# Kernel optimization log

Measured on AMD Instinct MI355X. Metric: run time of the kernel, lower is better.

The kernel has to match this reference:

```python
import jax, jax.numpy as jnp
import numpy as np

K_NEIGHBORS = 32  # nsample

def setup_inputs() -> dict:
    key = jax.random.key(0)
    ks = jax.random.split(key, 16)
    B, C, N = 4, 3, 4096
    def w(k, shape):
        return jax.random.normal(k, shape, dtype=jnp.float32) * 0.05
    inp = {"x": jax.random.normal(ks[0], (B, C, N), dtype=jnp.float32)}
    # three scale MLPs share shapes -> stack along leading scale axis (s=3)
    inp["sW0"] = w(ks[1], (3, 64, 3));    inp["sb0"] = w(ks[2], (3, 64))
    inp["sW1"] = w(ks[3], (3, 64, 64));   inp["sb1"] = w(ks[4], (3, 64))
    inp["sW2"] = w(ks[5], (3, 128, 64));  inp["sb2"] = w(ks[6], (3, 128))
    inp["gW0"] = w(ks[7], (256, 384));    inp["gb0"] = w(ks[8], (256,))
    inp["gW1"] = w(ks[9], (1024, 256));   inp["gb1"] = w(ks[10], (1024,))
    inp["mW0"] = w(ks[11], (256, 1024));  inp["mb0"] = w(ks[12], (256,))
    inp["mW1"] = w(ks[13], (128, 256));   inp["mb1"] = w(ks[14], (128,))
    return inp

def _knn_idx(x, k):
    # x: [B, 3, N] channels-first points; k nearest neighbors excluding self
    pts = jnp.swapaxes(x, 1, 2)                       # [B, N, 3]
    sq = jnp.sum(pts * pts, axis=-1)                  # [B, N]
    d = sq[:, :, None] + sq[:, None, :] - 2.0 * jnp.einsum('bnc,bmc->bnm', pts, pts)
    _, idx = jax.lax.top_k(-d, k + 1)                 # nearest first (self at 0)
    return idx[:, :, 1:]                              # [B, N, k]

def reference(x, sW0, sb0, sW1, sb1, sW2, sb2, gW0, gb0, gW1, gb1, mW0, mb0, mW1, mb1):
    B, C, N = x.shape
    # radius is unused by sample_and_group_knn -> all three scales share knn idx
    idx = _knn_idx(x, K_NEIGHBORS)                    # [B, N, K]
    # gather: per-batch x[:, idx[b]] -> [B, C, N, K]
    g = jax.vmap(lambda xf, i: xf[:, i])(x, idx)
    # three shared-weight 1x1-conv MLPs, batched over scale axis s
    h = jax.nn.relu(jnp.einsum('bcnk,soc->sbonk', g, sW0) + sb0[:, None, :, None, None])
    h = jax.nn.relu(jnp.einsum('sbcnk,soc->sbonk', h, sW1) + sb1[:, None, :, None, None])
    h = jax.nn.relu(jnp.einsum('sbcnk,soc->sbonk', h, sW2) + sb2[:, None, :, None, None])
    p = jnp.max(h, axis=-1)                           # [3, B, 128, N] max over neighbors
    point = jnp.moveaxis(p, 0, 1).reshape(B, 3 * p.shape[2], N)  # concat scales -> [B, 384, N]
    gf = jax.nn.relu(jnp.einsum('bcn,oc->bon', point, gW0) + gb0[None, :, None])
    gf = jax.nn.relu(jnp.einsum('bcn,oc->bon', gf, gW1) + gb1[None, :, None])     # [B,1024,N]
    msf = jax.nn.relu(jnp.einsum('bcn,oc->bon', gf, mW0) + mb0[None, :, None])
    msf = jax.nn.relu(jnp.einsum('bcn,oc->bon', msf, mW1) + mb1[None, :, None])   # [B,128,N]
    global_feature = jnp.max(gf, axis=-1)             # [B, 1024]
    return (global_feature, msf)
```

## Files before the change

### kernel.cpp

```cpp
#include <hip/hip_runtime.h>
#include <hip/hip_bf16.h>

#define NPTS 4096
#define KNN  32

typedef __attribute__((ext_vector_type(8))) short short8;
typedef __attribute__((ext_vector_type(4))) float floatx4;
typedef unsigned short u16x2 __attribute__((ext_vector_type(2)));

__device__ __forceinline__ unsigned short f2bf(float f) {
    unsigned u = __float_as_uint(f);
    u = (u + 0x7FFFu + ((u >> 16) & 1u)) >> 16;
    return (unsigned short)u;
}

__global__ __launch_bounds__(256) void prep_all(
    const float* __restrict__ x, float4* __restrict__ pts4,
    const float* __restrict__ gW0, const float* __restrict__ gW1,
    const float* __restrict__ mW0, const float* __restrict__ mW1,
    const float* __restrict__ sW1, const float* __restrict__ sW2,
    unsigned short* __restrict__ Wb0, unsigned short* __restrict__ Wb1,
    unsigned short* __restrict__ Wb2, unsigned short* __restrict__ Wb3,
    unsigned short* __restrict__ Wb4, unsigned short* __restrict__ Wb5)
{
    const int blk = blockIdx.x, t = threadIdx.x;
    if (blk < 64) {
        const int i = blk * 256 + t;
        const int b = i >> 12, n = i & (NPTS - 1);
        const float* xb = x + (size_t)b * 3 * NPTS;
        const float qx = xb[n], qy = xb[NPTS + n], qz = xb[2 * NPTS + n];
        pts4[i] = make_float4(qx, qy, qz, qx * qx + qy * qy + qz * qz);
    } else {
        const int wi = (blk - 64) * 256 + t;
        float v; unsigned short* dst;
        if (wi < 98304)       { v = gW0[wi];          dst = Wb0 + wi; }
        else if (wi < 360448) { v = gW1[wi - 98304];  dst = Wb1 + (wi - 98304); }
        else if (wi < 622592) { v = mW0[wi - 360448]; dst = Wb2 + (wi - 360448); }
        else if (wi < 655360) { v = mW1[wi - 622592]; dst = Wb3 + (wi - 622592); }
        else if (wi < 667648) { v = sW1[wi - 655360]; dst = Wb4 + (wi - 655360); }
        else                  { v = sW2[wi - 667648]; dst = Wb5 + (wi - 667648); }
        *dst = f2bf(v);
    }
}

__global__ __launch_bounds__(256) void knn_kernel19(const float4* __restrict__ pts4,
                                                    int* __restrict__ knn_out)
{
    __shared__ unsigned sredA[2][4], sredB[2][4];
    __shared__ unsigned minSA[256], minSB[256];
    __shared__ unsigned long long CA[256], CB[256];
    __shared__ unsigned ccnt2[2];

    const int t = threadIdx.x, wid = t >> 6, lane = t & 63;
    const int pr = blockIdx.x;
    const int b  = pr >> 11;
    const int qa = ((pr & 2047) << 1);
    const int qb = qa + 1;
    const float4* P = pts4 + ((size_t)b << 12);
    const float4 sA = P[qa];
    const float4 sB = P[qb];

    if (t < 2) ccnt2[t] = 0u;
    CA[t] = 0xFFFFFFFFFFFFFFFFULL;
    CB[t] = 0xFFFFFFFFFFFFFFFFULL;

    unsigned kA[16], kB[16];
    #pragma unroll
    for (int g = 0; g < 4; ++g) {
        float4 c0 = P[((g * 4 + 0) << 8) + t];
        float4 c1 = P[((g * 4 + 1) << 8) + t];
        float4 c2 = P[((g * 4 + 2) << 8) + t];
        float4 c3 = P[((g * 4 + 3) << 8) + t];
        float dA0 = (sA.w + c0.w) - 2.0f * (sA.x * c0.x + sA.y * c0.y + sA.z * c0.z);
        float dA1 = (sA.w + c1.w) - 2.0f * (sA.x * c1.x + sA.y * c1.y + sA.z * c1.z);
        float dA2 = (sA.w + c2.w) - 2.0f * (sA.x * c2.x + sA.y * c2.y + sA.z * c2.z);
        float dA3 = (sA.w + c3.w) - 2.0f * (sA.x * c3.x + sA.y * c3.y + sA.z * c3.z);
        float dB0 = (sB.w + c0.w) - 2.0f * (sB.x * c0.x + sB.y * c0.y + sB.z * c0.z);
        float dB1 = (sB.w + c1.w) - 2.0f * (sB.x * c1.x + sB.y * c1.y + sB.z * c1.z);
        float dB2 = (sB.w + c2.w) - 2.0f * (sB.x * c2.x + sB.y * c2.y + sB.z * c2.z);
        float dB3 = (sB.w + c3.w) - 2.0f * (sB.x * c3.x + sB.y * c3.y + sB.z * c3.z);
        unsigned uA0 = __float_as_uint(dA0), uA1 = __float_as_uint(dA1);
        unsigned uA2 = __float_as_uint(dA2), uA3 = __float_as_uint(dA3);
        unsigned uB0 = __float_as_uint(dB0), uB1 = __float_as_uint(dB1);
        unsigned uB2 = __float_as_uint(dB2), uB3 = __float_as_uint(dB3);
        kA[g * 4 + 0] = uA0 ^ (((unsigned)((int)uA0 >> 31)) | 0x80000000u);
        kA[g * 4 + 1] = uA1 ^ (((unsigned)((int)uA1 >> 31)) | 0x80000000u);
        kA[g * 4 + 2] = uA2 ^ (((unsigned)((int)uA2 >> 31)) | 0x80000000u);
        kA[g * 4 + 3] = uA3 ^ (((unsigned)((int)uA3 >> 31)) | 0x80000000u);
        kB[g * 4 + 0] = uB0 ^ (((unsigned)((int)uB0 >> 31)) | 0x80000000u);
        kB[g * 4 + 1] = uB1 ^ (((unsigned)((int)uB1 >> 31)) | 0x80000000u);
        kB[g * 4 + 2] = uB2 ^ (((unsigned)((int)uB2 >> 31)) | 0x80000000u);
        kB[g * 4 + 3] = uB3 ^ (((unsigned)((int)uB3 >> 31)) | 0x80000000u);
    }

    unsigned tmA = kA[0], tmB = kB[0];
    #pragma unroll
    for (int r = 1; r < 16; ++r) {
        tmA = (kA[r] < tmA) ? kA[r] : tmA;
        tmB = (kB[r] < tmB) ? kB[r] : tmB;
    }
    minSA[t] = tmA;
    minSB[t] = tmB;
    __syncthreads();

    unsigned mA = minSA[lane], mB = minSB[lane];
    {
        unsigned a1 = minSA[lane + 64], a2 = minSA[lane + 128], a3 = minSA[lane + 192];
        unsigned b1 = minSB[lane + 64], b2 = minSB[lane + 128], b3 = minSB[lane + 192];
        mA = (a1 < mA) ? a1 : mA;  a2 = (a3 < a2) ? a3 : a2;  mA = (a2 < mA) ? a2 : mA;
        mB = (b1 < mB) ? b1 : mB;  b2 = (b3 < b2) ? b3 : b2;  mB = (b2 < mB) ? b2 : mB;
    }

    const unsigned msA = mA >> 16, msB = mB >> 16;
    unsigned loA = 0u, hiA = 0xFFFFu, loB = 0u, hiB = 0xFFFFu;
    for (int i = 0; i < 16; ++i) {
        const unsigned midA = (loA + hiA) >> 1;
        const unsigned midB = (loB + hiB) >> 1;
        const unsigned cA = (unsigned)__popcll(__ballot(msA <= midA));
        const unsigned cB = (unsigned)__popcll(__ballot(msB <= midB));
        if (cA >= 33u) hiA = midA; else loA = midA + 1u;
        if (cB >= 33u) hiB = midB; else loB = midB + 1u;
    }
    const unsigned thrA = (hiA << 16) | 0xFFFFu;
    const unsigned thrB = (hiB << 16) | 0xFFFFu;

    #pragma unroll
    for (int r = 0; r < 16; ++r) {
        if (kA[r] <= thrA) {
            unsigned p = atomicAdd(&ccnt2[0], 1u);
            if (p < 256u)
                CA[p] = ((unsigned long long)kA[r] << 32) | (unsigned)((r << 8) + t);
        }
        if (kB[r] <= thrB) {
            unsigned p = atomicAdd(&ccnt2[1], 1u);
            if (p < 256u)
                CB[p] = ((unsigned long long)kB[r] << 32) | (unsigned)((r << 8) + t);
        }
    }
    __syncthreads();

    int ncA = (int)ccnt2[0];
    int ncB = (int)ccnt2[1];
    bool fell_back = false;
    if (ncA > 256 || ncB > 256) {
        fell_back = true;
        if (t < 2) ccnt2[t] = 0u;
        int pp = 0;
        auto countLE2 = [&](unsigned ta, unsigned tb, unsigned& ga, unsigned& gb) {
            unsigned ca = 0, cb = 0;
            #pragma unroll
            for (int r = 0; r < 16; ++r) {
                ca += (unsigned)__popcll(__ballot(kA[r] <= ta));
                cb += (unsigned)__popcll(__ballot(kB[r] <= tb));
            }
            if (lane == 0) { sredA[pp & 1][wid] = ca; sredB[pp & 1][wid] = cb; }
            __syncthreads();
            ga = sredA[pp & 1][0] + sredA[pp & 1][1] +
                 sredA[pp & 1][2] + sredA[pp & 1][3];
            gb = sredB[pp & 1][0] + sredB[pp & 1][1] +
                 sredB[pp & 1][2] + sredB[pp & 1][3];
            ++pp;
        };
        unsigned lo2A = 0x100u, hi2A = 0x1FEu, cHiA = 4096u;
        unsigned lo2B = 0x100u, hi2B = 0x1FEu, cHiB = 4096u;
        for (int it = 0; it < 8; ++it) {
            const unsigned mAe = (lo2A + hi2A) >> 1;
            const unsigned mBe = (lo2B + hi2B) >> 1;
            unsigned ga, gb;
            countLE2((mAe << 23) | 0x7FFFFFu, (mBe << 23) | 0x7FFFFFu, ga, gb);
            if (ga >= 33u) { hi2A = mAe; cHiA = ga; } else lo2A = mAe + 1u;
            if (gb >= 33u) { hi2B = mBe; cHiB = gb; } else lo2B = mBe + 1u;
        }
        unsigned loKA = lo2A << 23, hiKA = (lo2A << 23) | 0x7FFFFFu, cFA = cHiA;
        unsigned loKB = lo2B << 23, hiKB = (lo2B << 23) | 0x7FFFFFu, cFB = cHiB;
        while (((cFA > 256u) && (loKA < hiKA)) || ((cFB > 256u) && (loKB < hiKB))) {
            const bool nAx = (cFA > 256u) && (loKA < hiKA);
            const bool nBx = (cFB > 256u) && (loKB < hiKB);
            const unsigned mAk = nAx ? (loKA + ((hiKA - loKA) >> 1)) : hiKA;
            const unsigned mBk = nBx ? (loKB + ((hiKB - loKB) >> 1)) : hiKB;
            unsigned ga, gb;
            countLE2(mAk, mBk, ga, gb);
            if (nAx) { if (ga >= 33u) { hiKA = mAk; cFA = ga; } else loKA = mAk + 1u; }
            if (nBx) { if (gb >= 33u) { hiKB = mBk; cFB = gb; } else loKB = mBk + 1u; }
        }
        const unsigned tFA = hiKA, tFB = hiKB;
        #pragma unroll
        for (int r = 0; r < 16; ++r) {
            if (kA[r] <= tFA) {
                unsigned p = atomicAdd(&ccnt2[0], 1u);
                if (p < 256u)
                    CA[p] = ((unsigned long long)kA[r] << 32) | (unsigned)((r << 8) + t);
            }
            if (kB[r] <= tFB) {
                unsigned p = atomicAdd(&ccnt2[1], 1u);
                if (p < 256u)
                    CB[p] = ((unsigned long long)kB[r] << 32) | (unsigned)((r << 8) + t);
            }
        }
        __syncthreads();
        ncA = (int)ccnt2[0]; if (ncA > 256) ncA = 256;
        ncB = (int)ccnt2[1]; if (ncB > 256) ncB = 256;
    }

    if (!fell_back && ncA <= 64 && ncB <= 64) {
        if (t < 64) {
            const unsigned long long me = CA[t];
            int rank = 0;
            #pragma unroll
            for (int j = 0; j < 64; ++j) rank += (CA[j] < me) ? 1 : 0;
            if (rank >= 1 && rank <= KNN)
                knn_out[((size_t)((b << 12) + qa)) * KNN + (rank - 1)] =
                    (int)(me & 0xFFFFFFFFu);
        } else if (t < 128) {
            const int tb = t - 64;
            const unsigned long long me = CB[tb];
            int rank = 0;
            #pragma unroll
            for (int j = 0; j < 64; ++j) rank += (CB[j] < me) ? 1 : 0;
            if (rank >= 1 && rank <= KNN)
                knn_out[((size_t)((b << 12) + qb)) * KNN + (rank - 1)] =
                    (int)(me & 0xFFFFFFFFu);
        }
    } else {
        if (t < ncA) {
            const unsigned long long me = CA[t];
            int rank = 0;
            for (int j = 0; j < ncA; ++j) rank += (CA[j] < me) ? 1 : 0;
            if (rank >= 1 && rank <= KNN)
                knn_out[((size_t)((b << 12) + qa)) * KNN + (rank - 1)] =
                    (int)(me & 0xFFFFFFFFu);
        }
        if (t < ncB) {
            const unsigned long long me = CB[t];
            int rank = 0;
            for (int j = 0; j < ncB; ++j) rank += (CB[j] < me) ? 1 : 0;
            if (rank >= 1 && rank <= KNN)
                knn_out[((size_t)((b << 12) + qb)) * KNN + (rank - 1)] =
                    (int)(me & 0xFFFFFFFFu);
        }
    }
}

__global__ __launch_bounds__(256) void pointmlp_mfma(
    const float* __restrict__ x,
    const float* __restrict__ sW0, const float* __restrict__ sb0,
    const unsigned short* __restrict__ W1b, const float* __restrict__ sb1,
    const unsigned short* __restrict__ W2b, const float* __restrict__ sb2,
    unsigned short* __restrict__ F)
{
    __shared__ __align__(16) unsigned short W1s[64 * 72];
    __shared__ __align__(16) unsigned short W2s[128 * 72];
    __shared__ __align__(16) unsigned short h0T[32 * 72];
    __shared__ __align__(16) unsigned short h1T[32 * 72];
    __shared__ float W0s[192];
    __shared__ float b0s[64], b1s[64], b2s[128];
    __shared__ float pts[3 * 33];

    const int t = threadIdx.x;
    const int s = blockIdx.y;
    const int tile = blockIdx.x;
    const int b = tile >> 7;
    const int j0 = (tile & 127) << 5;
    const float* xb = x + (size_t)b * 3 * NPTS;

    if (t < 192) W0s[t] = sW0[s * 192 + t];
    if (t < 64) b0s[t] = sb0[s * 64 + t];
    if (t >= 64 && t < 128) b1s[t - 64] = sb1[s * 64 + (t - 64)];
    if (t < 128) b2s[t] = sb2[s * 128 + t];
    if (t < 96) { int c = t >> 5, p = t & 31; pts[c * 33 + p] = xb[c * NPTS + j0 + p]; }
    {
        const int o = t & 63, qq = t >> 6;
        const unsigned short* src = W1b + (size_t)s * 4096 + o * 64 + qq * 16;
        *(uint4*)&W1s[o * 72 + qq * 16]     = *(const uint4*)src;
        *(uint4*)&W1s[o * 72 + qq * 16 + 8] = *(const uint4*)(src + 8);
    }
    {
        const int o2 = t & 127, hh = t >> 7;
        const unsigned short* src = W2b + (size_t)s * 8192 + o2 * 64 + hh * 32;
        *(uint4*)&W2s[o2 * 72 + hh * 32]      = *(const uint4*)src;
        *(uint4*)&W2s[o2 * 72 + hh * 32 + 8]  = *(const uint4*)(src + 8);
        *(uint4*)&W2s[o2 * 72 + hh * 32 + 16] = *(const uint4*)(src + 16);
        *(uint4*)&W2s[o2 * 72 + hh * 32 + 24] = *(const uint4*)(src + 24);
    }
    __syncthreads();

    {
        const int p = t & 31, og = t >> 5;
        const float xx = pts[p], yy = pts[33 + p], zz = pts[66 + p];
        unsigned short hv[8];
        #pragma unroll
        for (int r = 0; r < 8; ++r) {
            const int o = og * 8 + r;
            float a = b0s[o] + W0s[o * 3] * xx + W0s[o * 3 + 1] * yy
                    + W0s[o * 3 + 2] * zz;
            hv[r] = f2bf(fmaxf(a, 0.0f));
        }
        *(uint4*)&h0T[p * 72 + og * 8] = *(const uint4*)hv;
    }
    __syncthreads();

    const int w = t >> 6, lane = t & 63, quad = lane >> 4, l15 = lane & 15;

    {
        #pragma unroll
        for (int ni = 0; ni < 2; ++ni) {
            floatx4 acc = (floatx4){0.f, 0.f, 0.f, 0.f};
            #pragma unroll
            for (int k0 = 0; k0 < 2; ++k0) {
                short8 aF = *(const short8*)&W1s[(w * 16 + l15) * 72 + k0 * 32 + quad * 8];
                short8 bF = *(const short8*)&h0T[(ni * 16 + l15) * 72 + k0 * 32 + quad * 8];
                acc = __builtin_amdgcn_mfma_f32_16x16x32_bf16(aF, bF, acc, 0, 0, 0);
            }
            const int m0 = w * 16 + quad * 4;
            const int p = ni * 16 + l15;
            ushort4 pk;
            pk.x = f2bf(fmaxf(acc[0] + b1s[m0 + 0], 0.f));
            pk.y = f2bf(fmaxf(acc[1] + b1s[m0 + 1], 0.f));
            pk.z = f2bf(fmaxf(acc[2] + b1s[m0 + 2], 0.f));
            pk.w = f2bf(fmaxf(acc[3] + b1s[m0 + 3], 0.f));
            *(ushort4*)&h1T[p * 72 + m0] = pk;
        }
    }
    __syncthreads();

    {
        #pragma unroll
        for (int mi = 0; mi < 2; ++mi) {
            const int m0 = (w * 2 + mi) * 16;
            #pragma unroll
            for (int ni = 0; ni < 2; ++ni) {
                floatx4 acc = (floatx4){0.f, 0.f, 0.f, 0.f};
                #pragma unroll
                for (int k0 = 0; k0 < 2; ++k0) {
                    short8 aF = *(const short8*)&W2s[(m0 + l15) * 72 + k0 * 32 + quad * 8];
                    short8 bF = *(const short8*)&h1T[(ni * 16 + l15) * 72 + k0 * 32 + quad * 8];
                    acc = __builtin_amdgcn_mfma_f32_16x16x32_bf16(aF, bF, acc, 0, 0, 0);
                }
                const int o2 = m0 + quad * 4;
                const int j = j0 + ni * 16 + l15;
                ushort4 pk;
                pk.x = f2bf(fmaxf(acc[0] + b2s[o2 + 0], 0.f));
                pk.y = f2bf(fmaxf(acc[1] + b2s[o2 + 1], 0.f));
                pk.z = f2bf(fmaxf(acc[2] + b2s[o2 + 2], 0.f));
                pk.w = f2bf(fmaxf(acc[3] + b2s[o2 + 3], 0.f));
                *(ushort4*)&F[((size_t)b * NPTS + j) * 384 + s * 128 + o2] = pk;
            }
        }
    }
}

__global__ __launch_bounds__(192) void maxgather_bf16(
    const unsigned short* __restrict__ F, const int* __restrict__ knn,
    unsigned short* __restrict__ pt)
{
    __shared__ int idxS[KNN];
    const int q = blockIdx.x;
    const int b = q >> 12;
    const int t = threadIdx.x;
    if (t < KNN) idxS[t] = knn[(size_t)q * KNN + t];
    __syncthreads();
    const unsigned short* Fb = F + (size_t)b * NPTS * 384 + t * 2;
    u16x2 m = (u16x2)0;
    #pragma unroll 8
    for (int k = 0; k < KNN; ++k) {
        u16x2 v = *(const u16x2*)(Fb + (size_t)idxS[k] * 384);
        m = __builtin_elementwise_max(m, v);
    }
    *(u16x2*)(pt + (size_t)q * 384 + t * 2) = m;
}

template<int DO_ROWMAX>
__global__ __launch_bounds__(256) void gemm_bf16(
    const unsigned short* __restrict__ Wb, const unsigned short* __restrict__ Bt,
    const float* __restrict__ bias, void* __restrict__ outp,
    float* __restrict__ gfeat, int M, int K)
{
    __shared__ __align__(16) unsigned short As[128 * 40];
    __shared__ __align__(16) unsigned short Bs[128 * 40];
    __shared__ float biasS[128];
    __shared__ int redI[128];

    const int t = threadIdx.x;
    const int b = blockIdx.z;
    const int m0 = blockIdx.x * 128;
    const int n0 = blockIdx.y * 128;
    if (t < 128) biasS[t] = bias[m0 + t];
    if (DO_ROWMAX && t < 128) redI[t] = 0;

    const int wave = t >> 6, lane = t & 63, quad = lane >> 4, l15 = lane & 15;
    const int wr = wave >> 1, wc = wave & 1;

    const int am = t & 127, akh = t >> 7;
    const unsigned short* Wp = Wb + (size_t)(m0 + am) * K + akh * 16;
    const int bn = t >> 2, bq = t & 3;
    const unsigned short* Bp = Bt + ((size_t)b * NPTS + n0) * K;

    floatx4 acc[16];
    #pragma unroll
    for (int i = 0; i < 16; ++i) acc[i] = (floatx4){0.f, 0.f, 0.f, 0.f};

    const int nk = K >> 5;
    for (int kt = 0; kt < nk; ++kt) {
        const int k0 = kt << 5;
        uint4 av0 = *(const uint4*)(Wp + k0);
        uint4 av1 = *(const uint4*)(Wp + k0 + 8);
        uint4 bv0 = *(const uint4*)(Bp + (size_t)bn * K + k0 + bq * 8);
        uint4 bv1 = *(const uint4*)(Bp + (size_t)(bn + 64) * K + k0 + bq * 8);
        __syncthreads();
        {
            uint4* dst = (uint4*)&As[am * 40 + akh * 16];
            dst[0] = av0;
            dst[1] = av1;
            *(uint4*)&Bs[bn * 40 + bq * 8] = bv0;
            *(uint4*)&Bs[(bn + 64) * 40 + bq * 8] = bv1;
        }
        __syncthreads();
        short8 af[4], bfv[4];
        #pragma unroll
        for (int i = 0; i < 4; ++i)
            af[i] = *(const short8*)&As[(wr * 64 + i * 16 + l15) * 40 + quad * 8];
        #pragma unroll
        for (int j = 0; j < 4; ++j)
            bfv[j] = *(const short8*)&Bs[(wc * 64 + j * 16 + l15) * 40 + quad * 8];
        #pragma unroll
        for (int i = 0; i < 4; ++i)
            #pragma unroll
            for (int j = 0; j < 4; ++j)
                acc[i * 4 + j] = __builtin_amdgcn_mfma_f32_16x16x32_bf16(
                    af[i], bfv[j], acc[i * 4 + j], 0, 0, 0);
    }

    #pragma unroll
    for (int i = 0; i < 4; ++i) {
        const int mbase = wr * 64 + i * 16 + quad * 4;
        float rm0 = 0.f, rm1 = 0.f, rm2 = 0.f, rm3 = 0.f;
        #pragma unroll
        for (int j = 0; j < 4; ++j) {
            const int n = n0 + wc * 64 + j * 16 + l15;
            float v0 = fmaxf(acc[i * 4 + j][0] + biasS[mbase + 0], 0.f);
            float v1 = fmaxf(acc[i * 4 + j][1] + biasS[mbase + 1], 0.f);
            float v2 = fmaxf(acc[i * 4 + j][2] + biasS[mbase + 2], 0.f);
            float v3 = fmaxf(acc[i * 4 + j][3] + biasS[mbase + 3], 0.f);
            if (DO_ROWMAX) {
                rm0 = fmaxf(rm0, v0); rm1 = fmaxf(rm1, v1);
                rm2 = fmaxf(rm2, v2); rm3 = fmaxf(rm3, v3);
            }
            ushort4 pk;
            pk.x = f2bf(v0); pk.y = f2bf(v1); pk.z = f2bf(v2); pk.w = f2bf(v3);
            *(ushort4*)((unsigned short*)outp +
                        ((size_t)b * NPTS + n) * M + m0 + mbase) = pk;
        }
        if (DO_ROWMAX) {
            atomicMax(&redI[mbase + 0], __float_as_int(rm0));
            atomicMax(&redI[mbase + 1], __float_as_int(rm1));
            atomicMax(&redI[mbase + 2], __float_as_int(rm2));
            atomicMax(&redI[mbase + 3], __float_as_int(rm3));
        }
    }
    if (DO_ROWMAX) {
        __syncthreads();
        if (t < 128)
            atomicMax((int*)&gfeat[(size_t)b * 1024 + m0 + t], redI[t]);
    }
}

__global__ __launch_bounds__(256) void fused_head(
    const unsigned short* __restrict__ Wb2, const unsigned short* __restrict__ Wb3,
    const float* __restrict__ mb0, const float* __restrict__ mb1,
    const unsigned short* __restrict__ gft, float* __restrict__ outp)
{
    __shared__ __align__(16) unsigned short As[256 * 40];
    __shared__ __align__(16) unsigned short Bs[64 * 40];
    __shared__ __align__(16) unsigned short H[64 * 264];
    __shared__ float b0s[256];
    __shared__ float b1s[128];

    const int t = threadIdx.x;
    const int n0 = blockIdx.x * 64;
    const int b = blockIdx.y;
    b0s[t] = mb0[t];
    if (t < 128) b1s[t] = mb1[t];

    const int wave = t >> 6, lane = t & 63, quad = lane >> 4, l15 = lane & 15;

    const unsigned short* Ap = Wb2 + (size_t)t * 1024;
    const int bn = t >> 2, bq = t & 3;
    const unsigned short* Bp = gft + ((size_t)b * NPTS + n0) * 1024;

    floatx4 acc[16];
    #pragma unroll
    for (int i = 0; i < 16; ++i) acc[i] = (floatx4){0.f, 0.f, 0.f, 0.f};

    for (int kt = 0; kt < 32; ++kt) {
        const int k0 = kt << 5;
        uint4 a0 = *(const uint4*)(Ap + k0);
        uint4 a1 = *(const uint4*)(Ap + k0 + 8);
        uint4 a2 = *(const uint4*)(Ap + k0 + 16);
        uint4 a3 = *(const uint4*)(Ap + k0 + 24);
        uint4 bv = *(const uint4*)(Bp + (size_t)bn * 1024 + k0 + bq * 8);
        __syncthreads();
        *(uint4*)&As[t * 40 + 0]  = a0;
        *(uint4*)&As[t * 40 + 8]  = a1;
        *(uint4*)&As[t * 40 + 16] = a2;
        *(uint4*)&As[t * 40 + 24] = a3;
        *(uint4*)&Bs[bn * 40 + bq * 8] = bv;
        __syncthreads();
        short8 af[4], bfv[4];
        #pragma unroll
        for (int i = 0; i < 4; ++i)
            af[i] = *(const short8*)&As[(wave * 64 + i * 16 + l15) * 40 + quad * 8];
        #pragma unroll
        for (int j = 0; j < 4; ++j)
            bfv[j] = *(const short8*)&Bs[(j * 16 + l15) * 40 + quad * 8];
        #pragma unroll
        for (int i = 0; i < 4; ++i)
            #pragma unroll
            for (int j = 0; j < 4; ++j)
                acc[i * 4 + j] = __builtin_amdgcn_mfma_f32_16x16x32_bf16(
                    af[i], bfv[j], acc[i * 4 + j], 0, 0, 0);
    }
    #pragma unroll
    for (int i = 0; i < 4; ++i) {
        const int mbase = wave * 64 + i * 16 + quad * 4;
        #pragma unroll
        for (int j = 0; j < 4; ++j) {
            const int nl = j * 16 + l15;
            ushort4 pk;
            pk.x = f2bf(fmaxf(acc[i * 4 + j][0] + b0s[mbase + 0], 0.f));
            pk.y = f2bf(fmaxf(acc[i * 4 + j][1] + b0s[mbase + 1], 0.f));
            pk.z = f2bf(fmaxf(acc[i * 4 + j][2] + b0s[mbase + 2], 0.f));
            pk.w = f2bf(fmaxf(acc[i * 4 + j][3] + b0s[mbase + 3], 0.f));
            *(ushort4*)&H[nl * 264 + mbase] = pk;
        }
    }

    floatx4 acc2[8];
    #pragma unroll
    for (int i = 0; i < 8; ++i) acc2[i] = (floatx4){0.f, 0.f, 0.f, 0.f};
    const int am2 = t & 127, ah = t >> 7;

    for (int kt = 0; kt < 8; ++kt) {
        const int k0 = kt << 5;
        uint4 a0 = *(const uint4*)(Wb3 + (size_t)am2 * 256 + k0 + ah * 16);
        uint4 a1 = *(const uint4*)(Wb3 + (size_t)am2 * 256 + k0 + ah * 16 + 8);
        __syncthreads();
        *(uint4*)&As[am2 * 40 + ah * 16]     = a0;
        *(uint4*)&As[am2 * 40 + ah * 16 + 8] = a1;
        __syncthreads();
        short8 af2[2], bf2[4];
        #pragma unroll
        for (int i = 0; i < 2; ++i)
            af2[i] = *(const short8*)&As[(wave * 32 + i * 16 + l15) * 40 + quad * 8];
        #pragma unroll
        for (int j = 0; j < 4; ++j)
            bf2[j] = *(const short8*)&H[(j * 16 + l15) * 264 + k0 + quad * 8];
        #pragma unroll
        for (int i = 0; i < 2; ++i)
            #pragma unroll
            for (int j = 0; j < 4; ++j)
                acc2[i * 4 + j] = __builtin_amdgcn_mfma_f32_16x16x32_bf16(
                    af2[i], bf2[j], acc2[i * 4 + j], 0, 0, 0);
    }
    #pragma unroll
    for (int i = 0; i < 2; ++i) {
        const int m2 = wave * 32 + i * 16 + quad * 4;
        #pragma unroll
        for (int j = 0; j < 4; ++j) {
            const int n = n0 + j * 16 + l15;
            float* o = outp + ((size_t)b * 128 + m2) * NPTS + n;
            o[0 * NPTS] = fmaxf(acc2[i * 4 + j][0] + b1s[m2 + 0], 0.f);
            o[1 * NPTS] = fmaxf(acc2[i * 4 + j][1] + b1s[m2 + 1], 0.f);
            o[2 * NPTS] = fmaxf(acc2[i * 4 + j][2] + b1s[m2 + 2], 0.f);
            o[3 * NPTS] = fmaxf(acc2[i * 4 + j][3] + b1s[m2 + 3], 0.f);
        }
    }
}

extern "C" void kernel_launch(void* const* d_in, const int* in_sizes, int n_in,
                              void* d_out, int out_size, void* d_ws, size_t ws_size,
                              hipStream_t stream)
{
    const float* x   = (const float*)d_in[0];
    const float* sW0 = (const float*)d_in[1];
    const float* sb0 = (const float*)d_in[2];
    const float* sW1 = (const float*)d_in[3];
    const float* sb1 = (const float*)d_in[4];
    const float* sW2 = (const float*)d_in[5];
    const float* sb2 = (const float*)d_in[6];
    const float* gW0 = (const float*)d_in[7];
    const float* gb0 = (const float*)d_in[8];
    const float* gW1 = (const float*)d_in[9];
    const float* gb1 = (const float*)d_in[10];
    const float* mW0 = (const float*)d_in[11];
    const float* mb0 = (const float*)d_in[12];
    const float* mW1 = (const float*)d_in[13];
    const float* mb1 = (const float*)d_in[14];
    float* outp = (float*)d_out;

    char* ws = (char*)d_ws;
    int*            idx     = (int*)(ws);
    float4*         pts4    = (float4*)(ws + 2097152u);
    unsigned short* Wb0     = (unsigned short*)(ws + 2359296u);
    unsigned short* Wb1     = (unsigned short*)(ws + 2555904u);
    unsigned short* Wb2     = (unsigned short*)(ws + 3080192u);
    unsigned short* Wb3     = (unsigned short*)(ws + 3604480u);
    unsigned short* Wb4     = (unsigned short*)(ws + 3670016u);
    unsigned short* Wb5     = (unsigned short*)(ws + 3694592u);
    unsigned short* F       = (unsigned short*)(ws + 4194304u);
    unsigned short* point_t = (unsigned short*)(ws + 18874368u);
    unsigned short* gf0t    = (unsigned short*)(ws + 33554432u);
    unsigned short* gft     = (unsigned short*)(ws + 50331648u);

    prep_all<<<dim3(2768), dim3(256), 0, stream>>>(
        x, pts4, gW0, gW1, mW0, mW1, sW1, sW2, Wb0, Wb1, Wb2, Wb3, Wb4, Wb5);
    knn_kernel19<<<dim3(8192), dim3(256), 0, stream>>>(pts4, idx);
    pointmlp_mfma<<<dim3(512, 3), dim3(256), 0, stream>>>(
        x, sW0, sb0, Wb4, sb1, Wb5, sb2, F);
    maxgather_bf16<<<dim3(16384), dim3(192), 0, stream>>>(F, idx, point_t);
    gemm_bf16<0><<<dim3(2, 32, 4), dim3(256), 0, stream>>>(
        Wb0, point_t, gb0, gf0t, nullptr, 256, 384);
    gemm_bf16<1><<<dim3(8, 32, 4), dim3(256), 0, stream>>>(
        Wb1, gf0t, gb1, gft, outp, 1024, 256);
    fused_head<<<dim3(64, 4), dim3(256), 0, stream>>>(
        Wb2, Wb3, mb0, mb1, gft, outp + 4096);
}
```

Baseline: 240.8 us.

## Fuse point MLP into KNN kernel launch via interleaved block roles

Merges the independent KNN and per-point MLP kernels into one launch, interleaving 3 MLP blocks among every 16 KNN blocks so both workloads run concurrently and one launch boundary disappears. The MLP path now reads W1/W2 fragments straight from global memory instead of staging them in shared memory, so all block roles fit in a shared 11.8KB buffer. In exchange, weight reads depend on cache hits, and the KNN blocks now allocate the union-sized shared buffer.

```diff
diff --git a/kernel.cpp b/kernel.cpp
--- a/kernel.cpp
+++ b/kernel.cpp
@@ -43,16 +43,122 @@
     }
 }
 
-__global__ __launch_bounds__(256) void knn_kernel19(const float4* __restrict__ pts4,
-                                                    int* __restrict__ knn_out)
+__global__ __launch_bounds__(256) void knn_pm_fused(
+    const float4* __restrict__ pts4, int* __restrict__ knn_out,
+    const float* __restrict__ x,
+    const float* __restrict__ sW0, const float* __restrict__ sb0,
+    const unsigned short* __restrict__ W1b, const float* __restrict__ sb1,
+    const unsigned short* __restrict__ W2b, const float* __restrict__ sb2,
+    unsigned short* __restrict__ F)
 {
-    __shared__ unsigned sredA[2][4], sredB[2][4];
-    __shared__ unsigned minSA[256], minSB[256];
-    __shared__ unsigned long long CA[256], CB[256];
-    __shared__ unsigned ccnt2[2];
-
-    const int t = threadIdx.x, wid = t >> 6, lane = t & 63;
-    const int pr = blockIdx.x;
+    __shared__ __align__(16) char smem[11776];
+
+    const int t = threadIdx.x;
+    const int grp = blockIdx.x / 19, rr = blockIdx.x % 19;
+
+    if (rr < 3) {
+        const int pm_id = grp * 3 + rr;
+        unsigned short* h0T = (unsigned short*)(smem);
+        unsigned short* h1T = (unsigned short*)(smem + 4608);
+        float* W0s = (float*)(smem + 9216);
+        float* b0s = (float*)(smem + 9984);
+        float* b1s = (float*)(smem + 10240);
+        float* b2s = (float*)(smem + 10496);
+        float* pts = (float*)(smem + 11008);
+
+        const int s = pm_id / 512;
+        const int tile = pm_id % 512;
+        const int b = tile >> 7;
+        const int j0 = (tile & 127) << 5;
+        const float* xb = x + (size_t)b * 3 * NPTS;
+
+        if (t < 192) W0s[t] = sW0[s * 192 + t];
+        if (t < 64) b0s[t] = sb0[s * 64 + t];
+        if (t >= 64 && t < 128) b1s[t - 64] = sb1[s * 64 + (t - 64)];
+        if (t < 128) b2s[t] = sb2[s * 128 + t];
+        if (t < 96) { int c = t >> 5, p = t & 31; pts[c * 33 + p] = xb[c * NPTS + j0 + p]; }
+        __syncthreads();
+
+        {
+            const int p = t & 31, og = t >> 5;
+            const float xx = pts[p], yy = pts[33 + p], zz = pts[66 + p];
+            unsigned short hv[8];
+            #pragma unroll
+            for (int r = 0; r < 8; ++r) {
+                const int o = og * 8 + r;
+                float a = b0s[o] + W0s[o * 3] * xx + W0s[o * 3 + 1] * yy
+                        + W0s[o * 3 + 2] * zz;
+                hv[r] = f2bf(fmaxf(a, 0.0f));
+            }
+            *(uint4*)&h0T[p * 72 + og * 8] = *(const uint4*)hv;
+        }
+        __syncthreads();
+
+        const int w = t >> 6, lane = t & 63, quad = lane >> 4, l15 = lane & 15;
+        const unsigned short* W1g = W1b + (size_t)s * 4096;
+        const unsigned short* W2g = W2b + (size_t)s * 8192;
+
+        {
+            #pragma unroll
+            for (int ni = 0; ni < 2; ++ni) {
+                floatx4 acc = (floatx4){0.f, 0.f, 0.f, 0.f};
+                #pragma unroll
+                for (int k0 = 0; k0 < 2; ++k0) {
+                    short8 aF = *(const short8*)(W1g + (w * 16 + l15) * 64 +
+                                                 k0 * 32 + quad * 8);
+                    short8 bF = *(const short8*)&h0T[(ni * 16 + l15) * 72 + k0 * 32 + quad * 8];
+                    acc = __builtin_amdgcn_mfma_f32_16x16x32_bf16(aF, bF, acc, 0, 0, 0);
+                }
+                const int m0 = w * 16 + quad * 4;
+                const int p = ni * 16 + l15;
+                ushort4 pk;
+                pk.x = f2bf(fmaxf(acc[0] + b1s[m0 + 0], 0.f));
+                pk.y = f2bf(fmaxf(acc[1] + b1s[m0 + 1], 0.f));
+                pk.z = f2bf(fmaxf(acc[2] + b1s[m0 + 2], 0.f));
+                pk.w = f2bf(fmaxf(acc[3] + b1s[m0 + 3], 0.f));
+                *(ushort4*)&h1T[p * 72 + m0] = pk;
+            }
+        }
+        __syncthreads();
+
+        {
+            #pragma unroll
+            for (int mi = 0; mi < 2; ++mi) {
+                const int m0 = (w * 2 + mi) * 16;
+                #pragma unroll
+                for (int ni = 0; ni < 2; ++ni) {
+                    floatx4 acc = (floatx4){0.f, 0.f, 0.f, 0.f};
+                    #pragma unroll
+                    for (int k0 = 0; k0 < 2; ++k0) {
+                        short8 aF = *(const short8*)(W2g + (m0 + l15) * 64 +
+                                                     k0 * 32 + quad * 8);
+                        short8 bF = *(const short8*)&h1T[(ni * 16 + l15) * 72 + k0 * 32 + quad * 8];
+                        acc = __builtin_amdgcn_mfma_f32_16x16x32_bf16(aF, bF, acc, 0, 0, 0);
+                    }
+                    const int o2 = m0 + quad * 4;
+                    const int j = j0 + ni * 16 + l15;
+                    ushort4 pk;
+                    pk.x = f2bf(fmaxf(acc[0] + b2s[o2 + 0], 0.f));
+                    pk.y = f2bf(fmaxf(acc[1] + b2s[o2 + 1], 0.f));
+                    pk.z = f2bf(fmaxf(acc[2] + b2s[o2 + 2], 0.f));
+                    pk.w = f2bf(fmaxf(acc[3] + b2s[o2 + 3], 0.f));
+                    *(ushort4*)&F[((size_t)b * NPTS + j) * 384 + s * 128 + o2] = pk;
+                }
+            }
+        }
+        return;
+    }
+
+    unsigned (*sredA)[4]   = (unsigned(*)[4])(smem);
+    unsigned (*sredB)[4]   = (unsigned(*)[4])(smem + 32);
+    unsigned* minSA        = (unsigned*)(smem + 64);
+    unsigned* minSB        = (unsigned*)(smem + 1088);
+    unsigned long long* CA = (unsigned long long*)(smem + 2112);
+    unsigned long long* CB = (unsigned long long*)(smem + 4160);
+    unsigned* ccnt2        = (unsigned*)(smem + 6208);
+
+    const int wid = t >> 6, lane = t & 63;
+    const int pr = grp * 16 + (rr - 3);
     const int b  = pr >> 11;
     const int qa = ((pr & 2047) << 1);
     const int qb = qa + 1;
@@ -241,114 +347,6 @@
     }
 }
 
-__global__ __launch_bounds__(256) void pointmlp_mfma(
-    const float* __restrict__ x,
-    const float* __restrict__ sW0, const float* __restrict__ sb0,
-    const unsigned short* __restrict__ W1b, const float* __restrict__ sb1,
-    const unsigned short* __restrict__ W2b, const float* __restrict__ sb2,
-    unsigned short* __restrict__ F)
-{
-    __shared__ __align__(16) unsigned short W1s[64 * 72];
-    __shared__ __align__(16) unsigned short W2s[128 * 72];
-    __shared__ __align__(16) unsigned short h0T[32 * 72];
-    __shared__ __align__(16) unsigned short h1T[32 * 72];
-    __shared__ float W0s[192];
-    __shared__ float b0s[64], b1s[64], b2s[128];
-    __shared__ float pts[3 * 33];
-
-    const int t = threadIdx.x;
-    const int s = blockIdx.y;
-    const int tile = blockIdx.x;
-    const int b = tile >> 7;
-    const int j0 = (tile & 127) << 5;
-    const float* xb = x + (size_t)b * 3 * NPTS;
-
-    if (t < 192) W0s[t] = sW0[s * 192 + t];
-    if (t < 64) b0s[t] = sb0[s * 64 + t];
-    if (t >= 64 && t < 128) b1s[t - 64] = sb1[s * 64 + (t - 64)];
-    if (t < 128) b2s[t] = sb2[s * 128 + t];
-    if (t < 96) { int c = t >> 5, p = t & 31; pts[c * 33 + p] = xb[c * NPTS + j0 + p]; }
-    {
-        const int o = t & 63, qq = t >> 6;
-        const unsigned short* src = W1b + (size_t)s * 4096 + o * 64 + qq * 16;
-        *(uint4*)&W1s[o * 72 + qq * 16]     = *(const uint4*)src;
-        *(uint4*)&W1s[o * 72 + qq * 16 + 8] = *(const uint4*)(src + 8);
-    }
-    {
-        const int o2 = t & 127, hh = t >> 7;
-        const unsigned short* src = W2b + (size_t)s * 8192 + o2 * 64 + hh * 32;
-        *(uint4*)&W2s[o2 * 72 + hh * 32]      = *(const uint4*)src;
-        *(uint4*)&W2s[o2 * 72 + hh * 32 + 8]  = *(const uint4*)(src + 8);
-        *(uint4*)&W2s[o2 * 72 + hh * 32 + 16] = *(const uint4*)(src + 16);
-        *(uint4*)&W2s[o2 * 72 + hh * 32 + 24] = *(const uint4*)(src + 24);
-    }
-    __syncthreads();
-
-    {
-        const int p = t & 31, og = t >> 5;
-        const float xx = pts[p], yy = pts[33 + p], zz = pts[66 + p];
-        unsigned short hv[8];
-        #pragma unroll
-        for (int r = 0; r < 8; ++r) {
-            const int o = og * 8 + r;
-            float a = b0s[o] + W0s[o * 3] * xx + W0s[o * 3 + 1] * yy
-                    + W0s[o * 3 + 2] * zz;
-            hv[r] = f2bf(fmaxf(a, 0.0f));
-        }
-        *(uint4*)&h0T[p * 72 + og * 8] = *(const uint4*)hv;
-    }
-    __syncthreads();
-
-    const int w = t >> 6, lane = t & 63, quad = lane >> 4, l15 = lane & 15;
-
-    {
-        #pragma unroll
-        for (int ni = 0; ni < 2; ++ni) {
-            floatx4 acc = (floatx4){0.f, 0.f, 0.f, 0.f};
-            #pragma unroll
-            for (int k0 = 0; k0 < 2; ++k0) {
-                short8 aF = *(const short8*)&W1s[(w * 16 + l15) * 72 + k0 * 32 + quad * 8];
-                short8 bF = *(const short8*)&h0T[(ni * 16 + l15) * 72 + k0 * 32 + quad * 8];
-                acc = __builtin_amdgcn_mfma_f32_16x16x32_bf16(aF, bF, acc, 0, 0, 0);
-            }
-            const int m0 = w * 16 + quad * 4;
-            const int p = ni * 16 + l15;
-            ushort4 pk;
-            pk.x = f2bf(fmaxf(acc[0] + b1s[m0 + 0], 0.f));
-            pk.y = f2bf(fmaxf(acc[1] + b1s[m0 + 1], 0.f));
-            pk.z = f2bf(fmaxf(acc[2] + b1s[m0 + 2], 0.f));
-            pk.w = f2bf(fmaxf(acc[3] + b1s[m0 + 3], 0.f));
-            *(ushort4*)&h1T[p * 72 + m0] = pk;
-        }
-    }
-    __syncthreads();
-
-    {
-        #pragma unroll
-        for (int mi = 0; mi < 2; ++mi) {
-            const int m0 = (w * 2 + mi) * 16;
-            #pragma unroll
-            for (int ni = 0; ni < 2; ++ni) {
-                floatx4 acc = (floatx4){0.f, 0.f, 0.f, 0.f};
-                #pragma unroll
-                for (int k0 = 0; k0 < 2; ++k0) {
-                    short8 aF = *(const short8*)&W2s[(m0 + l15) * 72 + k0 * 32 + quad * 8];
-                    short8 bF = *(const short8*)&h1T[(ni * 16 + l15) * 72 + k0 * 32 + quad * 8];
-                    acc = __builtin_amdgcn_mfma_f32_16x16x32_bf16(aF, bF, acc, 0, 0, 0);
-                }
-                const int o2 = m0 + quad * 4;
-                const int j = j0 + ni * 16 + l15;
-                ushort4 pk;
-                pk.x = f2bf(fmaxf(acc[0] + b2s[o2 + 0], 0.f));
-                pk.y = f2bf(fmaxf(acc[1] + b2s[o2 + 1], 0.f));
-                pk.z = f2bf(fmaxf(acc[2] + b2s[o2 + 2], 0.f));
-                pk.w = f2bf(fmaxf(acc[3] + b2s[o2 + 3], 0.f));
-                *(ushort4*)&F[((size_t)b * NPTS + j) * 384 + s * 128 + o2] = pk;
-            }
-        }
-    }
-}
-
 __global__ __launch_bounds__(192) void maxgather_bf16(
     const unsigned short* __restrict__ F, const int* __restrict__ knn,
     unsigned short* __restrict__ pt)
@@ -613,9 +611,8 @@
 
     prep_all<<<dim3(2768), dim3(256), 0, stream>>>(
         x, pts4, gW0, gW1, mW0, mW1, sW1, sW2, Wb0, Wb1, Wb2, Wb3, Wb4, Wb5);
-    knn_kernel19<<<dim3(8192), dim3(256), 0, stream>>>(pts4, idx);
-    pointmlp_mfma<<<dim3(512, 3), dim3(256), 0, stream>>>(
-        x, sW0, sb0, Wb4, sb1, Wb5, sb2, F);
+    knn_pm_fused<<<dim3(9728), dim3(256), 0, stream>>>(
+        pts4, idx, x, sW0, sb0, Wb4, sb1, Wb5, sb2, F);
     maxgather_bf16<<<dim3(16384), dim3(192), 0, stream>>>(F, idx, point_t);
     gemm_bf16<0><<<dim3(2, 32, 4), dim3(256), 0, stream>>>(
         Wb0, point_t, gb0, gf0t, nullptr, 256, 384);
```

Result: faster. 233.9 us (-2.9%).
